# Optimization experiments

Measured on AMD Instinct MI355X. Metric: run time of the kernel, lower is better.

## Reference

```python
import jax, jax.numpy as jnp
import numpy as np

N_NODES = 100000
N_EDGES = 1600000
DIM_IN, DIM_HID, DIM_OUT = 64, 128, 40


def setup_inputs() -> dict:
    key = jax.random.key(0)
    ks = jax.random.split(key, 6)
    x = jax.random.normal(ks[0], (N_NODES, DIM_IN), dtype=jnp.float32)
    edge_index = jax.random.randint(ks[1], (2, N_EDGES), 0, N_NODES, dtype=jnp.int64)
    s_in = 1.0 / np.sqrt(DIM_IN)
    s_hid = 1.0 / np.sqrt(DIM_HID)
    W1l = jax.random.normal(ks[2], (DIM_HID, DIM_IN), dtype=jnp.float32) * s_in
    W1r = jax.random.normal(ks[3], (DIM_HID, DIM_IN), dtype=jnp.float32) * s_in
    b1 = jnp.zeros((DIM_HID,), dtype=jnp.float32)
    W2l = jax.random.normal(ks[4], (DIM_OUT, DIM_HID), dtype=jnp.float32) * s_hid
    W2r = jax.random.normal(ks[5], (DIM_OUT, DIM_HID), dtype=jnp.float32) * s_hid
    b2 = jnp.zeros((DIM_OUT,), dtype=jnp.float32)
    return {"x": x, "edge_index": edge_index, "W1l": W1l, "b1": b1,
            "W1r": W1r, "W2l": W2l, "b2": b2, "W2r": W2r}


def _sage_conv(h, src, dst, Wl, bl, Wr, n_nodes):
    # mean aggregation of source-node features into target nodes
    msg = h[src]                                      # [E, d]
    agg = jax.ops.segment_sum(msg, dst, num_segments=n_nodes)
    cnt = jax.ops.segment_sum(jnp.ones((src.shape[0],), h.dtype), dst,
                              num_segments=n_nodes)
    agg = agg / jnp.maximum(cnt, 1.0)[:, None]        # [N, d]
    # PyG SAGEConv: lin_l(agg) + bias + lin_r(x) (root weight, no bias)
    return agg @ Wl.T + bl + h @ Wr.T


def reference(x, edge_index, W1l, b1, W1r, W2l, b2, W2r):
    src, dst = edge_index[0], edge_index[1]
    n = x.shape[0]
    h = _sage_conv(x, src, dst, W1l, b1, W1r, n)
    h = jax.nn.relu(h)
    out = _sage_conv(h, src, dst, W2l, b2, W2r, n)
    return jax.nn.log_softmax(out, axis=-1)
```

## Files before the change

### kernel.cpp

```cpp
#include <hip/hip_runtime.h>
#include <math.h>

#define NN 100000
#define DI 64
#define DH 128
#define DO 40

#define NBUCK 512
#define NPB 196
#define CAP 3712
#define CAPP 5120
#define EPB 4096
#define TPB_S 512
#define KE (EPB / TPB_S)

typedef __attribute__((ext_vector_type(8))) short bf16x8;
typedef __attribute__((ext_vector_type(4))) float f32x4;
typedef __attribute__((ext_vector_type(2))) float f32x2;

__device__ __forceinline__ unsigned short bf16r(float a) {
    unsigned u = __float_as_uint(a);
    u = (u + 0x7FFF + ((u >> 16) & 1)) >> 16;
    return (unsigned short)u;
}
__device__ __forceinline__ unsigned bf16pair(float a, float b) {
    return (unsigned)bf16r(a) | ((unsigned)bf16r(b) << 16);
}
__device__ __forceinline__ float bflo(unsigned u) { return __uint_as_float(u << 16); }
__device__ __forceinline__ float bfhi(unsigned u) { return __uint_as_float(u & 0xFFFF0000u); }

__global__ __launch_bounds__(TPB_S) void setup_scatter_kernel(
        const float* __restrict__ x, const float* __restrict__ W1l,
        const float* __restrict__ W1r, const float* __restrict__ W2l,
        const float* __restrict__ W2r,
        unsigned* __restrict__ xb, unsigned short* __restrict__ xgs,
        unsigned short* __restrict__ WB1,
        unsigned short* __restrict__ WB2, unsigned* __restrict__ p2,
        const int* __restrict__ src, const int* __restrict__ dst,
        int* __restrict__ bcur, int* __restrict__ eb,
        int nbe, int E, int N) {
    __shared__ int h[NBUCK];
    int t = threadIdx.x;
    if ((int)blockIdx.x < nbe) {
        if (t < NBUCK) h[t] = 0;
        __syncthreads();
        int base = blockIdx.x * EPB;
        int end = base + EPB; if (end > E) end = E;
        int dloc[KE];
#pragma unroll
        for (int k = 0; k < KE; k++) {
            int i = base + t + k * TPB_S;
            dloc[k] = (i < end) ? dst[i] : -1;
        }
#pragma unroll
        for (int k = 0; k < KE; k++)
            if (dloc[k] >= 0) atomicAdd(&h[(unsigned)dloc[k] / NPB], 1);
        __syncthreads();
        if (t < NBUCK) {
            int v = h[t];
            h[t] = v ? (atomicAdd(&bcur[t], v) + t * CAP) : 0;
        }
        __syncthreads();
#pragma unroll
        for (int k = 0; k < KE; k++) {
            int d = dloc[k];
            if (d >= 0) {
                unsigned bk = (unsigned)d / NPB;
                int local = d - (int)bk * NPB;
                int pos = atomicAdd(&h[bk], 1);
                eb[pos] = (local << 17) | src[base + t + k * TPB_S];
            }
        }
    } else {
        int idx = (blockIdx.x - nbe) * TPB_S + t;
        if (idx < (N + 1) * 32) {
            if (idx < N * 32) {
                float2 f = ((const float2*)x)[idx];
                xb[idx] = bf16pair(f.x, f.y);
                xgs[idx] = (unsigned short)
                    __builtin_amdgcn_cvt_pk_fp8_f32(f.x, f.y, 0u, false);
            } else {
                xb[idx] = 0;
                xgs[idx] = 0;
            }
        }
        if (idx < 16384) {
            int j = idx & 7, lane = (idx >> 3) & 63, ks = (idx >> 9) & 3, nt = idx >> 11;
            int k = ks * 32 + (lane >> 4) * 8 + j;
            int n = nt * 16 + (lane & 15);
            float v = (k < DI) ? W1l[n * DI + k] : W1r[n * DI + (k - DI)];
            WB1[idx] = bf16r(v);
        }
        if (idx >= 16384 && idx < 16384 + 10240) {
            int idx2 = idx - 16384;
            int j = idx2 & 7, lane = (idx2 >> 3) & 63, ks = (idx2 >> 9) & 3, nt = idx2 >> 11;
            int k = ks * 32 + (lane >> 4) * 8 + j;
            int n = nt * 16 + (lane & 15);
            float v = (n < DO) ? W2l[n * DH + k] : W2r[(n - DO) * DH + k];
            WB2[idx2] = bf16r(v);
        }
        if (idx < 10) p2[(size_t)N * 10 + idx] = 0;
    }
}

__global__ __launch_bounds__(256) void bucket_fill_kernel(const int* __restrict__ eb,
                                                          const int* __restrict__ bend,
                                                          int* __restrict__ rowptr,
                                                          int* __restrict__ cntg,
                                                          float* __restrict__ inv,
                                                          int* __restrict__ col, int N) {
    __shared__ int scnt[256];
    __shared__ int scur[256];
    __shared__ int sbase[256];
    int b = blockIdx.x, t = threadIdx.x;
    int ebeg = b * CAP, eend = ebeg + bend[b];
    scnt[t] = 0;
    __syncthreads();
    for (int i = ebeg + t; i < eend; i += 256)
        atomicAdd(&scnt[eb[i] >> 17], 1);
    __syncthreads();
    int myc = scnt[t];
    int pc = (myc + 7) & ~7;
    scnt[t] = pc;
    __syncthreads();
    for (int off = 1; off < 256; off <<= 1) {
        int tmp = (t >= off) ? scnt[t - off] : 0;
        __syncthreads();
        scnt[t] += tmp;
        __syncthreads();
    }
    int excl = scnt[t] - pc;
    int base = b * CAPP + excl;
    int node = b * NPB + t;
    if (t < NPB && node < N) {
        rowptr[node] = base;
        cntg[node] = myc;
        inv[node] = 1.0f / (float)(myc > 0 ? myc : 1);
    }
    scur[t] = base;
    sbase[t] = base;
    __syncthreads();
    for (int i = ebeg + t; i < eend; i += 256) {
        int pk = eb[i];
        int pos = atomicAdd(&scur[pk >> 17], 1);
        col[pos] = pk & 0x1FFFF;
    }
    __syncthreads();
    if (t < NPB) {
        int bs = sbase[t];
        for (int i = myc; i < pc; i++) col[bs + i] = NN;
    }
}

__global__ __launch_bounds__(256) void agg_gemm12_kernel(
        const unsigned* __restrict__ xb, const unsigned short* __restrict__ xgs,
        const int* __restrict__ rowptr,
        const int* __restrict__ cnt, const float* __restrict__ inv,
        const int* __restrict__ col,
        const unsigned short* __restrict__ WB1, const float* __restrict__ b1,
        const unsigned short* __restrict__ WB2, const float* __restrict__ b2,
        unsigned* __restrict__ p2, unsigned short* __restrict__ selfpb, int N) {
    __shared__ unsigned short sh[64][136];
    int t = threadIdx.x;
    int w = t >> 6, lane = t & 63;
    int lw = w * 16;
    int g8 = (t >> 3) & 7;
    int chunk = t & 7;
    int rbase = blockIdx.x * 64 + lw;

#pragma unroll
    for (int it = 0; it < 2; ++it) {
        int lr = lw + g8 + it * 8;
        int n = blockIdx.x * 64 + lr;
        bool valid = (n < N);
        int ne = valid ? n : NN;
        float a[8];
#pragma unroll
        for (int j = 0; j < 8; j++) a[j] = 0.f;
        float invn = 0.f;
        if (valid) {
            int beg = rowptr[n], deg = cnt[n];
            int degp = (deg + 3) & ~3;
            for (int i = 0; i < degp; i += 4) {
                int4 c = *(const int4*)(col + beg + i);
                uint2 g0 = *(const uint2*)(xgs + (size_t)c.x * 32 + chunk * 4);
                uint2 g1 = *(const uint2*)(xgs + (size_t)c.y * 32 + chunk * 4);
                uint2 g2 = *(const uint2*)(xgs + (size_t)c.z * 32 + chunk * 4);
                uint2 g3 = *(const uint2*)(xgs + (size_t)c.w * 32 + chunk * 4);
                f32x2 d;
                d = __builtin_amdgcn_cvt_pk_f32_fp8(g0.x, false); a[0] += d.x; a[1] += d.y;
                d = __builtin_amdgcn_cvt_pk_f32_fp8(g0.x, true);  a[2] += d.x; a[3] += d.y;
                d = __builtin_amdgcn_cvt_pk_f32_fp8(g0.y, false); a[4] += d.x; a[5] += d.y;
                d = __builtin_amdgcn_cvt_pk_f32_fp8(g0.y, true);  a[6] += d.x; a[7] += d.y;
                d = __builtin_amdgcn_cvt_pk_f32_fp8(g1.x, false); a[0] += d.x; a[1] += d.y;
                d = __builtin_amdgcn_cvt_pk_f32_fp8(g1.x, true);  a[2] += d.x; a[3] += d.y;
                d = __builtin_amdgcn_cvt_pk_f32_fp8(g1.y, false); a[4] += d.x; a[5] += d.y;
                d = __builtin_amdgcn_cvt_pk_f32_fp8(g1.y, true);  a[6] += d.x; a[7] += d.y;
                d = __builtin_amdgcn_cvt_pk_f32_fp8(g2.x, false); a[0] += d.x; a[1] += d.y;
                d = __builtin_amdgcn_cvt_pk_f32_fp8(g2.x, true);  a[2] += d.x; a[3] += d.y;
                d = __builtin_amdgcn_cvt_pk_f32_fp8(g2.y, false); a[4] += d.x; a[5] += d.y;
                d = __builtin_amdgcn_cvt_pk_f32_fp8(g2.y, true);  a[6] += d.x; a[7] += d.y;
                d = __builtin_amdgcn_cvt_pk_f32_fp8(g3.x, false); a[0] += d.x; a[1] += d.y;
                d = __builtin_amdgcn_cvt_pk_f32_fp8(g3.x, true);  a[2] += d.x; a[3] += d.y;
                d = __builtin_amdgcn_cvt_pk_f32_fp8(g3.y, false); a[4] += d.x; a[5] += d.y;
                d = __builtin_amdgcn_cvt_pk_f32_fp8(g3.y, true);  a[6] += d.x; a[7] += d.y;
            }
            invn = inv[n];
        }
        uint4 u = *(const uint4*)(xb + (size_t)ne * 32 + chunk * 4);
        uint4 o;
        o.x = bf16pair(a[0] * invn, a[1] * invn);
        o.y = bf16pair(a[2] * invn, a[3] * invn);
        o.z = bf16pair(a[4] * invn, a[5] * invn);
        o.w = bf16pair(a[6] * invn, a[7] * invn);
        *(uint4*)&sh[lr][chunk * 8] = o;
        *(uint4*)&sh[lr][64 + chunk * 8] = u;
    }
    asm volatile("" ::: "memory");

    int quad = lane >> 4, m = lane & 15;
    f32x4 acc[8];
#pragma unroll
    for (int nt = 0; nt < 8; nt++) acc[nt] = (f32x4)(0.f);
#pragma unroll
    for (int ks = 0; ks < 4; ks++) {
        bf16x8 a = *(const bf16x8*)(&sh[lw + m][ks * 32 + quad * 8]);
#pragma unroll
        for (int nt = 0; nt < 8; nt++) {
            bf16x8 b = *(const bf16x8*)(WB1 + ((size_t)(nt * 4 + ks) * 64 + lane) * 8);
            acc[nt] = __builtin_amdgcn_mfma_f32_16x16x32_bf16(a, b, acc[nt], 0, 0, 0);
        }
    }
    asm volatile("" ::: "memory");
#pragma unroll
    for (int nt = 0; nt < 8; nt++) {
        int colj = nt * 16 + m;
        float bj = b1[colj];
#pragma unroll
        for (int r = 0; r < 4; r++) {
            sh[lw + quad * 4 + r][colj] = bf16r(fmaxf(acc[nt][r] + bj, 0.f));
        }
    }
    asm volatile("" ::: "memory");

    f32x4 acc2[5];
#pragma unroll
    for (int nt = 0; nt < 5; nt++) acc2[nt] = (f32x4)(0.f);
#pragma unroll
    for (int ks = 0; ks < 4; ks++) {
        bf16x8 a = *(const bf16x8*)(&sh[lw + m][ks * 32 + quad * 8]);
#pragma unroll
        for (int nt = 0; nt < 5; nt++) {
            bf16x8 b = *(const bf16x8*)(WB2 + ((size_t)(nt * 4 + ks) * 64 + lane) * 8);
            acc2[nt] = __builtin_amdgcn_mfma_f32_16x16x32_bf16(a, b, acc2[nt], 0, 0, 0);
        }
    }
    asm volatile("" ::: "memory");
    float* stw = (float*)&sh[lw][0];
#pragma unroll
    for (int nt = 0; nt < 5; nt++) {
        int colj = nt * 16 + m;
#pragma unroll
        for (int r = 0; r < 4; r++) {
            int row = rbase + quad * 4 + r;
            float v = acc2[nt][r];
            if (colj < 40) {
                stw[(quad * 4 + r) * 41 + colj] = v;
            } else if (row < N) {
                selfpb[(size_t)row * 40 + (colj - 40)] = bf16r(v + b2[colj - 40]);
            }
        }
    }
    asm volatile("" ::: "memory");
    for (int i = lane; i < 160; i += 64) {
        int lr = i / 10, dw = i - lr * 10;
        int grow = rbase + lr;
        if (grow < N) {
            float v0 = stw[lr * 41 + dw * 4 + 0], v1 = stw[lr * 41 + dw * 4 + 1];
            float v2 = stw[lr * 41 + dw * 4 + 2], v3 = stw[lr * 41 + dw * 4 + 3];
            unsigned u = __builtin_amdgcn_cvt_pk_fp8_f32(v0, v1, 0u, false);
            u = __builtin_amdgcn_cvt_pk_fp8_f32(v2, v3, u, true);
            p2[(size_t)grow * 10 + dw] = u;
        }
    }
}

__global__ void agg2_softmax_kernel(const unsigned* __restrict__ p2,
                                    const unsigned short* __restrict__ selfpb,
                                    const int* __restrict__ rowptr,
                                    const int* __restrict__ cnt,
                                    const float* __restrict__ inv,
                                    const int* __restrict__ col,
                                    float* __restrict__ out, int N) {
    int n = (blockIdx.x * 256 + threadIdx.x) >> 3;
    int chunk = threadIdx.x & 7;
    if (n >= N) return;
    int beg = rowptr[n], deg = cnt[n];
    int degp = (deg + 7) & ~7;
    bool vc = (chunk < 5);
    float a[8];
#pragma unroll
    for (int j = 0; j < 8; j++) a[j] = 0.f;
    for (int i = 0; i < degp; i += 8) {
        int ss[8];
#pragma unroll
        for (int k = 0; k < 8; k++) ss[k] = col[beg + i + k];
        if (vc) {
            uint2 uu[8];
#pragma unroll
            for (int k = 0; k < 8; k++)
                uu[k] = *(const uint2*)(p2 + (size_t)ss[k] * 10 + chunk * 2);
#pragma unroll
            for (int k = 0; k < 8; k++) {
                f32x2 d;
                d = __builtin_amdgcn_cvt_pk_f32_fp8(uu[k].x, false); a[0] += d.x; a[1] += d.y;
                d = __builtin_amdgcn_cvt_pk_f32_fp8(uu[k].x, true);  a[2] += d.x; a[3] += d.y;
                d = __builtin_amdgcn_cvt_pk_f32_fp8(uu[k].y, false); a[4] += d.x; a[5] += d.y;
                d = __builtin_amdgcn_cvt_pk_f32_fp8(uu[k].y, true);  a[6] += d.x; a[7] += d.y;
            }
        }
    }
    float invn = inv[n];
    float v[8];
    if (vc) {
        uint4 sv = *(const uint4*)(selfpb + (size_t)n * 40 + chunk * 8);
        v[0] = a[0] * invn + bflo(sv.x); v[1] = a[1] * invn + bfhi(sv.x);
        v[2] = a[2] * invn + bflo(sv.y); v[3] = a[3] * invn + bfhi(sv.y);
        v[4] = a[4] * invn + bflo(sv.z); v[5] = a[5] * invn + bfhi(sv.z);
        v[6] = a[6] * invn + bflo(sv.w); v[7] = a[7] * invn + bfhi(sv.w);
    } else {
#pragma unroll
        for (int j = 0; j < 8; j++) v[j] = 0.f;
    }
    float mv = -INFINITY;
    if (vc) {
#pragma unroll
        for (int j = 0; j < 8; j++) mv = fmaxf(mv, v[j]);
    }
#pragma unroll
    for (int off = 1; off <= 4; off <<= 1) mv = fmaxf(mv, __shfl_xor(mv, off, 8));
    float es = 0.f;
    if (vc) {
#pragma unroll
        for (int j = 0; j < 8; j++) es += expf(v[j] - mv);
    }
#pragma unroll
    for (int off = 1; off <= 4; off <<= 1) es += __shfl_xor(es, off, 8);
    if (vc) {
        float ls = mv + logf(es);
        float4 o0, o1;
        o0.x = v[0] - ls; o0.y = v[1] - ls; o0.z = v[2] - ls; o0.w = v[3] - ls;
        o1.x = v[4] - ls; o1.y = v[5] - ls; o1.z = v[6] - ls; o1.w = v[7] - ls;
        *(float4*)(out + (size_t)n * DO + chunk * 8) = o0;
        *(float4*)(out + (size_t)n * DO + chunk * 8 + 4) = o1;
    }
}

extern "C" void kernel_launch(void* const* d_in, const int* in_sizes, int n_in,
                              void* d_out, int out_size, void* d_ws, size_t ws_size,
                              hipStream_t stream) {
    const float* x   = (const float*)d_in[0];
    const int*  ei   = (const int*)d_in[1];
    const float* W1l = (const float*)d_in[2];
    const float* b1  = (const float*)d_in[3];
    const float* W1r = (const float*)d_in[4];
    const float* W2l = (const float*)d_in[5];
    const float* b2  = (const float*)d_in[6];
    const float* W2r = (const float*)d_in[7];
    float* out = (float*)d_out;

    const int E = in_sizes[1] / 2;
    const int N = NN;
    const int* src = ei;
    const int* dst = ei + E;
    const int nbe = (E + EPB - 1) / EPB;
    const int nsetup = ((N + 1) * 32 + TPB_S - 1) / TPB_S;

    size_t off = 0;
    auto alloc = [&](size_t nf) { size_t o = off; off += (nf + 63) & ~(size_t)63; return o; };
    size_t o_bcur   = alloc(NBUCK);
    size_t o_eb     = alloc((size_t)NBUCK * CAP);
    size_t o_col    = alloc((size_t)NBUCK * CAPP + 64);
    size_t o_rowptr = alloc(N);
    size_t o_cnt    = alloc(N);
    size_t o_inv    = alloc(N);
    size_t o_xb     = alloc((size_t)(N + 1) * 32);
    size_t o_xg     = alloc((size_t)(N + 1) * 16);
    size_t o_p2     = alloc((size_t)(N + 1) * 10);
    size_t o_selfp  = alloc((size_t)N * 20);
    size_t o_wb1    = alloc(16384 / 2);
    size_t o_wb2    = alloc(10240 / 2);
    (void)ws_size;

    float* ws = (float*)d_ws;
    int* bcur   = (int*)(ws + o_bcur);
    int* eb     = (int*)(ws + o_eb);
    int* col    = (int*)(ws + o_col);
    int* rowptr = (int*)(ws + o_rowptr);
    int* cnt    = (int*)(ws + o_cnt);
    float* inv  = ws + o_inv;
    unsigned* xb = (unsigned*)(ws + o_xb);
    unsigned short* xgs = (unsigned short*)(ws + o_xg);
    unsigned* p2 = (unsigned*)(ws + o_p2);
    unsigned short* selfpb = (unsigned short*)(ws + o_selfp);
    unsigned short* WB1 = (unsigned short*)(ws + o_wb1);
    unsigned short* WB2 = (unsigned short*)(ws + o_wb2);

    hipMemsetAsync(bcur, 0, NBUCK * sizeof(int), stream);

    setup_scatter_kernel<<<nbe + nsetup, TPB_S, 0, stream>>>(
        x, W1l, W1r, W2l, W2r, xb, xgs, WB1, WB2, p2, src, dst, bcur, eb, nbe, E, N);

    bucket_fill_kernel<<<NBUCK, 256, 0, stream>>>(eb, bcur, rowptr, cnt, inv, col, N);

    agg_gemm12_kernel<<<(N + 63) / 64, 256, 0, stream>>>(
        xb, xgs, rowptr, cnt, inv, col, WB1, b1, WB2, b2, p2, selfpb, N);

    agg2_softmax_kernel<<<(N * 8 + 255) / 256, 256, 0, stream>>>(p2, selfpb, rowptr, cnt, inv, col, out, N);
}
```

Baseline: 194.2 us.

## Fuse bucket CSR fill into layer-1 aggregation kernel with 64-node buckets

Bucket size changes to 64 nodes so each aggregation block owns exactly one bucket. The separate bucket_fill kernel is removed. The aggregation kernel now builds the per-node column lists in shared memory, reads neighbours from LDS, and writes the CSR to global memory for layer 2. This saves one kernel launch and a global round trip of the column array for layer 1. In exchange it adds more LDS per block, more histogram buckets in the scatter kernel, and a fixed per-bucket capacity that could overflow on skewed degree distributions.

```diff
diff --git a/kernel.cpp b/kernel.cpp
--- a/kernel.cpp
+++ b/kernel.cpp
@@ -6,10 +6,10 @@
 #define DH 128
 #define DO 40
 
-#define NBUCK 512
-#define NPB 196
-#define CAP 3712
-#define CAPP 5120
+#define NPB 64
+#define NBUCK 1563
+#define CAP 1408
+#define COLCAP 1856
 #define EPB 4096
 #define TPB_S 512
 #define KE (EPB / TPB_S)
@@ -42,7 +42,7 @@
     __shared__ int h[NBUCK];
     int t = threadIdx.x;
     if ((int)blockIdx.x < nbe) {
-        if (t < NBUCK) h[t] = 0;
+        for (int i = t; i < NBUCK; i += TPB_S) h[i] = 0;
         __syncthreads();
         int base = blockIdx.x * EPB;
         int end = base + EPB; if (end > E) end = E;
@@ -54,19 +54,19 @@
         }
 #pragma unroll
         for (int k = 0; k < KE; k++)
-            if (dloc[k] >= 0) atomicAdd(&h[(unsigned)dloc[k] / NPB], 1);
+            if (dloc[k] >= 0) atomicAdd(&h[(unsigned)dloc[k] >> 6], 1);
         __syncthreads();
-        if (t < NBUCK) {
-            int v = h[t];
-            h[t] = v ? (atomicAdd(&bcur[t], v) + t * CAP) : 0;
+        for (int i = t; i < NBUCK; i += TPB_S) {
+            int v = h[i];
+            h[i] = v ? (atomicAdd(&bcur[i], v) + i * CAP) : 0;
         }
         __syncthreads();
 #pragma unroll
         for (int k = 0; k < KE; k++) {
             int d = dloc[k];
             if (d >= 0) {
-                unsigned bk = (unsigned)d / NPB;
-                int local = d - (int)bk * NPB;
+                unsigned bk = (unsigned)d >> 6;
+                int local = d & 63;
                 int pos = atomicAdd(&h[bk], 1);
                 eb[pos] = (local << 17) | src[base + t + k * TPB_S];
             }
@@ -103,75 +103,75 @@
     }
 }
 
-__global__ __launch_bounds__(256) void bucket_fill_kernel(const int* __restrict__ eb,
-                                                          const int* __restrict__ bend,
-                                                          int* __restrict__ rowptr,
-                                                          int* __restrict__ cntg,
-                                                          float* __restrict__ inv,
-                                                          int* __restrict__ col, int N) {
-    __shared__ int scnt[256];
-    __shared__ int scur[256];
-    __shared__ int sbase[256];
-    int b = blockIdx.x, t = threadIdx.x;
-    int ebeg = b * CAP, eend = ebeg + bend[b];
-    scnt[t] = 0;
-    __syncthreads();
-    for (int i = ebeg + t; i < eend; i += 256)
-        atomicAdd(&scnt[eb[i] >> 17], 1);
-    __syncthreads();
-    int myc = scnt[t];
-    int pc = (myc + 7) & ~7;
-    scnt[t] = pc;
-    __syncthreads();
-    for (int off = 1; off < 256; off <<= 1) {
-        int tmp = (t >= off) ? scnt[t - off] : 0;
-        __syncthreads();
-        scnt[t] += tmp;
-        __syncthreads();
-    }
-    int excl = scnt[t] - pc;
-    int base = b * CAPP + excl;
-    int node = b * NPB + t;
-    if (t < NPB && node < N) {
-        rowptr[node] = base;
-        cntg[node] = myc;
-        inv[node] = 1.0f / (float)(myc > 0 ? myc : 1);
-    }
-    scur[t] = base;
-    sbase[t] = base;
-    __syncthreads();
-    for (int i = ebeg + t; i < eend; i += 256) {
-        int pk = eb[i];
-        int pos = atomicAdd(&scur[pk >> 17], 1);
-        col[pos] = pk & 0x1FFFF;
-    }
-    __syncthreads();
-    if (t < NPB) {
-        int bs = sbase[t];
-        for (int i = myc; i < pc; i++) col[bs + i] = NN;
-    }
-}
-
 __global__ __launch_bounds__(256) void agg_gemm12_kernel(
         const unsigned* __restrict__ xb, const unsigned short* __restrict__ xgs,
-        const int* __restrict__ rowptr,
-        const int* __restrict__ cnt, const float* __restrict__ inv,
-        const int* __restrict__ col,
+        const int* __restrict__ eb, const int* __restrict__ bend,
+        int* __restrict__ rowptr, int* __restrict__ cntg, float* __restrict__ invg,
+        int* __restrict__ colg,
         const unsigned short* __restrict__ WB1, const float* __restrict__ b1,
         const unsigned short* __restrict__ WB2, const float* __restrict__ b2,
         unsigned* __restrict__ p2, unsigned short* __restrict__ selfpb, int N) {
     __shared__ unsigned short sh[64][136];
+    __shared__ __align__(16) int col_l[COLCAP];
+    __shared__ int scnt[64], sbase[64], scur[64];
+    __shared__ int stot;
     int t = threadIdx.x;
+    int b = blockIdx.x;
+    int cnt_b = bend[b];
+    size_t ebeg = (size_t)b * CAP;
+
+    if (t < 64) scnt[t] = 0;
+    __syncthreads();
+    for (int i = t; i < cnt_b; i += 256)
+        atomicAdd(&scnt[eb[ebeg + i] >> 17], 1);
+    __syncthreads();
+    if (t < 64) {
+        int c = scnt[t];
+        int pc = (c + 7) & ~7;
+        int scan = pc;
+#pragma unroll
+        for (int off = 1; off < 64; off <<= 1) {
+            int u = __shfl_up(scan, off);
+            if (t >= off) scan += u;
+        }
+        int base = scan - pc;
+        sbase[t] = base;
+        scur[t] = base;
+        if (t == 63) stot = scan;
+        int node = b * 64 + t;
+        if (node < N) {
+            rowptr[node] = b * COLCAP + base;
+            cntg[node] = c;
+            invg[node] = 1.0f / (float)(c > 0 ? c : 1);
+        }
+    }
+    __syncthreads();
+    for (int i = t; i < cnt_b; i += 256) {
+        int pk = eb[ebeg + i];
+        int pos = atomicAdd(&scur[pk >> 17], 1);
+        col_l[pos] = pk & 0x1FFFF;
+    }
+    __syncthreads();
+    if (t < 64) {
+        int c = scnt[t], pc = (c + 7) & ~7, base = sbase[t];
+        for (int i = c; i < pc; i++) col_l[base + i] = NN;
+    }
+    __syncthreads();
+    {
+        int tot = stot;
+        for (int i = t; i < tot; i += 256)
+            colg[(size_t)b * COLCAP + i] = col_l[i];
+    }
+
     int w = t >> 6, lane = t & 63;
     int lw = w * 16;
     int g8 = (t >> 3) & 7;
     int chunk = t & 7;
-    int rbase = blockIdx.x * 64 + lw;
-
+    int rbase = b * 64 + lw;
 #pragma unroll
     for (int it = 0; it < 2; ++it) {
         int lr = lw + g8 + it * 8;
-        int n = blockIdx.x * 64 + lr;
+        int n = b * 64 + lr;
         bool valid = (n < N);
         int ne = valid ? n : NN;
         float a[8];
@@ -179,14 +179,14 @@
         for (int j = 0; j < 8; j++) a[j] = 0.f;
         float invn = 0.f;
         if (valid) {
-            int beg = rowptr[n], deg = cnt[n];
+            int beg = sbase[lr], deg = scnt[lr];
             int degp = (deg + 3) & ~3;
             for (int i = 0; i < degp; i += 4) {
-                int4 c = *(const int4*)(col + beg + i);
-                uint2 g0 = *(const uint2*)(xgs + (size_t)c.x * 32 + chunk * 4);
-                uint2 g1 = *(const uint2*)(xgs + (size_t)c.y * 32 + chunk * 4);
-                uint2 g2 = *(const uint2*)(xgs + (size_t)c.z * 32 + chunk * 4);
-                uint2 g3 = *(const uint2*)(xgs + (size_t)c.w * 32 + chunk * 4);
+                int4 c4 = *(const int4*)(col_l + beg + i);
+                uint2 g0 = *(const uint2*)(xgs + (size_t)c4.x * 32 + chunk * 4);
+                uint2 g1 = *(const uint2*)(xgs + (size_t)c4.y * 32 + chunk * 4);
+                uint2 g2 = *(const uint2*)(xgs + (size_t)c4.z * 32 + chunk * 4);
+                uint2 g3 = *(const uint2*)(xgs + (size_t)c4.w * 32 + chunk * 4);
                 f32x2 d;
                 d = __builtin_amdgcn_cvt_pk_f32_fp8(g0.x, false); a[0] += d.x; a[1] += d.y;
                 d = __builtin_amdgcn_cvt_pk_f32_fp8(g0.x, true);  a[2] += d.x; a[3] += d.y;
@@ -205,7 +205,7 @@
                 d = __builtin_amdgcn_cvt_pk_f32_fp8(g3.y, false); a[4] += d.x; a[5] += d.y;
                 d = __builtin_amdgcn_cvt_pk_f32_fp8(g3.y, true);  a[6] += d.x; a[7] += d.y;
             }
-            invn = inv[n];
+            invn = 1.0f / (float)(deg > 0 ? deg : 1);
         }
         uint4 u = *(const uint4*)(xb + (size_t)ne * 32 + chunk * 4);
         uint4 o;
@@ -227,8 +227,8 @@
         bf16x8 a = *(const bf16x8*)(&sh[lw + m][ks * 32 + quad * 8]);
 #pragma unroll
         for (int nt = 0; nt < 8; nt++) {
-            bf16x8 b = *(const bf16x8*)(WB1 + ((size_t)(nt * 4 + ks) * 64 + lane) * 8);
-            acc[nt] = __builtin_amdgcn_mfma_f32_16x16x32_bf16(a, b, acc[nt], 0, 0, 0);
+            bf16x8 bb = *(const bf16x8*)(WB1 + ((size_t)(nt * 4 + ks) * 64 + lane) * 8);
+            acc[nt] = __builtin_amdgcn_mfma_f32_16x16x32_bf16(a, bb, acc[nt], 0, 0, 0);
         }
     }
     asm volatile("" ::: "memory");
@@ -251,8 +251,8 @@
         bf16x8 a = *(const bf16x8*)(&sh[lw + m][ks * 32 + quad * 8]);
 #pragma unroll
         for (int nt = 0; nt < 5; nt++) {
-            bf16x8 b = *(const bf16x8*)(WB2 + ((size_t)(nt * 4 + ks) * 64 + lane) * 8);
-            acc2[nt] = __builtin_amdgcn_mfma_f32_16x16x32_bf16(a, b, acc2[nt], 0, 0, 0);
+            bf16x8 bb = *(const bf16x8*)(WB2 + ((size_t)(nt * 4 + ks) * 64 + lane) * 8);
+            acc2[nt] = __builtin_amdgcn_mfma_f32_16x16x32_bf16(a, bb, acc2[nt], 0, 0, 0);
         }
     }
     asm volatile("" ::: "memory");
@@ -380,7 +380,7 @@
     auto alloc = [&](size_t nf) { size_t o = off; off += (nf + 63) & ~(size_t)63; return o; };
     size_t o_bcur   = alloc(NBUCK);
     size_t o_eb     = alloc((size_t)NBUCK * CAP);
-    size_t o_col    = alloc((size_t)NBUCK * CAPP + 64);
+    size_t o_colg   = alloc((size_t)NBUCK * COLCAP + 64);
     size_t o_rowptr = alloc(N);
     size_t o_cnt    = alloc(N);
     size_t o_inv    = alloc(N);
@@ -395,7 +395,7 @@
     float* ws = (float*)d_ws;
     int* bcur   = (int*)(ws + o_bcur);
     int* eb     = (int*)(ws + o_eb);
-    int* col    = (int*)(ws + o_col);
+    int* colg   = (int*)(ws + o_colg);
     int* rowptr = (int*)(ws + o_rowptr);
     int* cnt    = (int*)(ws + o_cnt);
     float* inv  = ws + o_inv;
@@ -411,10 +411,10 @@
     setup_scatter_kernel<<<nbe + nsetup, TPB_S, 0, stream>>>(
         x, W1l, W1r, W2l, W2r, xb, xgs, WB1, WB2, p2, src, dst, bcur, eb, nbe, E, N);
 
-    bucket_fill_kernel<<<NBUCK, 256, 0, stream>>>(eb, bcur, rowptr, cnt, inv, col, N);
-
-    agg_gemm12_kernel<<<(N + 63) / 64, 256, 0, stream>>>(
-        xb, xgs, rowptr, cnt, inv, col, WB1, b1, WB2, b2, p2, selfpb, N);
-
-    agg2_softmax_kernel<<<(N * 8 + 255) / 256, 256, 0, stream>>>(p2, selfpb, rowptr, cnt, inv, col, out, N);
-}
+    agg_gemm12_kernel<<<NBUCK, 256, 0, stream>>>(
+        xb, xgs, eb, bcur, rowptr, cnt, inv, colg,
+        WB1, b1, WB2, b2, p2, selfpb, N);
+
+    agg2_softmax_kernel<<<(N * 8 + 255) / 256, 256, 0, stream>>>(
+        p2, selfpb, rowptr, cnt, inv, colg, out, N);
+}
```

After: 196.0 us. No clear change (+1.0%).
